# Performance work log

Measured on AMD Instinct MI355X. Metric: run time of the kernel, lower is better.

## Reference

```python
import jax, jax.numpy as jnp
import numpy as np

# Matcher weights (Deformable-DETR defaults used by SimPLR-style repos)
COST_CLASS, COST_BBOX, COST_GIOU = 2.0, 5.0, 2.0
ALPHA, GAMMA = 0.25, 2.0  # focal cost hyperparams
EPS = 1e-8


def box_cxcywh_to_xyxy(b):
    cx, cy, w, h = jnp.split(b, 4, axis=-1)
    return jnp.concatenate([cx - 0.5 * w, cy - 0.5 * h, cx + 0.5 * w, cy + 0.5 * h], axis=-1)


def generalized_box_iou(b1, b2):
    # b1 [Q,4], b2 [T,4] in xyxy -> [Q,T]
    area1 = (b1[:, 2] - b1[:, 0]) * (b1[:, 3] - b1[:, 1])
    area2 = (b2[:, 2] - b2[:, 0]) * (b2[:, 3] - b2[:, 1])
    lt = jnp.maximum(b1[:, None, :2], b2[None, :, :2])
    rb = jnp.minimum(b1[:, None, 2:], b2[None, :, 2:])
    wh = jnp.clip(rb - lt, 0.0)
    inter = wh[..., 0] * wh[..., 1]
    union = area1[:, None] + area2[None, :] - inter
    iou = inter / union
    lt2 = jnp.minimum(b1[:, None, :2], b2[None, :, :2])
    rb2 = jnp.maximum(b1[:, None, 2:], b2[None, :, 2:])
    wh2 = jnp.clip(rb2 - lt2, 0.0)
    hull = wh2[..., 0] * wh2[..., 1]
    return iou - (hull - union) / hull


def cost_matrix(logits, boxes, tgt_ids, tgt_boxes):
    # per-image: logits [Q,C], boxes [Q,4] cxcywh, tgt_ids [T], tgt_boxes [T,4]
    prob = jax.nn.sigmoid(logits)
    neg = (1.0 - ALPHA) * (prob ** GAMMA) * (-jnp.log(1.0 - prob + EPS))
    pos = ALPHA * ((1.0 - prob) ** GAMMA) * (-jnp.log(prob + EPS))
    cost_class = pos[:, tgt_ids] - neg[:, tgt_ids]                    # [Q,T]
    cost_bbox = jnp.abs(boxes[:, None, :] - tgt_boxes[None, :, :]).sum(-1)  # L1 cdist [Q,T]
    cost_giou = -generalized_box_iou(box_cxcywh_to_xyxy(boxes), box_cxcywh_to_xyxy(tgt_boxes))
    return COST_BBOX * cost_bbox + COST_CLASS * cost_class + COST_GIOU * cost_giou


def lsa(cost):
    # Hungarian (Jonker-Volgenant / e-maxx shortest augmenting path), minimizes.
    # cost [n, m] with n <= m; returns col4row: column assigned to each row.
    n, m = cost.shape
    u = np.zeros(n + 1)
    v = np.zeros(m + 1)
    p = np.zeros(m + 1, dtype=np.int64)   # p[j] = row matched to col j (1-based), 0 = free
    way = np.zeros(m + 1, dtype=np.int64)
    for i in range(1, n + 1):
        p[0] = i
        j0 = 0
        minv = np.full(m + 1, np.inf)
        used = np.zeros(m + 1, dtype=bool)
        while True:
            used[j0] = True
            i0 = p[j0]
            free = ~used
            free[0] = False
            cur = cost[i0 - 1] - u[i0] - v[1:]
            better = np.zeros(m + 1, dtype=bool)
            better[1:] = free[1:] & (cur < minv[1:])
            minv[better] = cur[better[1:]]
            way[better] = j0
            cand = np.where(free[1:], minv[1:], np.inf)
            j1 = int(np.argmin(cand)) + 1
            delta = cand[j1 - 1]
            u[p[used]] += delta
            v[used] -= delta
            minv[free] -= delta
            j0 = j1
            if p[j0] == 0:
                break
        while j0 != 0:
            j1 = way[j0]
            p[j0] = p[j1]
            j0 = j1
    col4row = np.zeros(n, dtype=np.int64)
    for j in range(1, m + 1):
        if p[j] > 0:
            col4row[p[j] - 1] = j - 1
    return col4row


_batched_cost = jax.jit(jax.vmap(cost_matrix, in_axes=(0, 0, 0, 0)))


def setup_inputs() -> dict:
    key = jax.random.key(0)
    k1, k2, k3, k4 = jax.random.split(key, 4)
    bs, nq, nc, nt = 32, 900, 1203, 100
    return {
        "pred_logits": jax.random.normal(k1, (bs, nq, nc), dtype=jnp.float32),
        "pred_boxes": jax.random.uniform(k2, (bs, nq, 4), dtype=jnp.float32),
        "tgt_labels": jax.random.randint(k3, (bs, nt), 0, nc, dtype=jnp.int64),
        "tgt_boxes": jax.random.uniform(k4, (bs, nt, 4), dtype=jnp.float32),
    }


def reference(pred_logits, pred_boxes, tgt_labels, tgt_boxes):
    # Cost blocks [bs, Q, T] (identical to the per-image diagonal blocks of the
    # torch code's [bs, Q, sum_T] view, which are the only parts used).
    C = _batched_cost(pred_logits, pred_boxes, tgt_labels, tgt_boxes)
    Cn = np.asarray(jax.device_get(C))
    rows, cols = [], []
    for b in range(Cn.shape[0]):
        col4row = lsa(Cn[b].T)          # [T]: matched query index per target
        order = np.argsort(col4row)     # scipy returns row indices sorted ascending
        rows.append(col4row[order])     # index_i: selected prediction indices
        cols.append(order)              # index_j: corresponding target indices
    pred_idx = jnp.asarray(np.stack(rows), dtype=jnp.int64)  # [bs, T]
    tgt_idx = jnp.asarray(np.stack(cols), dtype=jnp.int64)   # [bs, T]
    return C, pred_idx, tgt_idx
```

## Files before the change

### kernel.cpp

```cpp
#include <hip/hip_runtime.h>
#include <math.h>

#define BS 32
#define NQ 900
#define NC 1203
#define NT 100
#define SLOTS 15
#define K8 8
#define JBLK 512
#define NW 8

__device__ float g_CT[(size_t)BS * NT * NQ];
__device__ unsigned long long g_topk[(size_t)BS * NT * K8];

__device__ __forceinline__ unsigned long long packf(float f, int col) {
    unsigned k = __float_as_uint(f);
    k = (k & 0x80000000u) ? ~k : (k | 0x80000000u);
    return ((unsigned long long)k << 32) | (unsigned)col;
}
__device__ __forceinline__ float unpack_val(unsigned long long p) {
    unsigned k = (unsigned)(p >> 32);
    unsigned bits = (k & 0x80000000u) ? (k ^ 0x80000000u) : ~k;
    return __uint_as_float(bits);
}
__device__ __forceinline__ int unpack_col(unsigned long long p) {
    return (int)(p & 0xFFFFFFFFu);
}

__global__ __launch_bounds__(128) void cost_kernel(
    const float* __restrict__ logits, const float* __restrict__ boxes,
    const int* __restrict__ tlabels, const float* __restrict__ tboxes,
    float* __restrict__ C)
{
    int bq = blockIdx.x;
    int b = bq / NQ, q = bq % NQ;
    int t = threadIdx.x;

    const float* pb = boxes + (size_t)(b * NQ + q) * 4;
    float pcx = pb[0], pcy = pb[1], pw = pb[2], ph = pb[3];

    if (t < NT) {
        int id = tlabels[b * NT + t];
        float x = logits[(size_t)(b * NQ + q) * NC + id];
        float prob = 1.0f / (1.0f + expf(-x));
        float neg = 0.75f * (prob * prob) * (-logf(1.0f - prob + 1e-8f));
        float pos = 0.25f * ((1.0f - prob) * (1.0f - prob)) * (-logf(prob + 1e-8f));
        float cclass = pos - neg;

        const float* tb = tboxes + (size_t)(b * NT + t) * 4;
        float tcx = tb[0], tcy = tb[1], tw = tb[2], th = tb[3];
        float cbbox = fabsf(pcx - tcx) + fabsf(pcy - tcy) + fabsf(pw - tw) + fabsf(ph - th);

        float p0 = pcx - 0.5f * pw, p1 = pcy - 0.5f * ph;
        float p2 = pcx + 0.5f * pw, p3 = pcy + 0.5f * ph;
        float t0 = tcx - 0.5f * tw, t1 = tcy - 0.5f * th;
        float t2 = tcx + 0.5f * tw, t3 = tcy + 0.5f * th;
        float area1 = (p2 - p0) * (p3 - p1);
        float area2 = (t2 - t0) * (t3 - t1);
        float ltx = fmaxf(p0, t0), lty = fmaxf(p1, t1);
        float rbx = fminf(p2, t2), rby = fminf(p3, t3);
        float wx = fmaxf(rbx - ltx, 0.0f), wy = fmaxf(rby - lty, 0.0f);
        float inter = wx * wy;
        float uni = area1 + area2 - inter;
        float iou = inter / uni;
        float l2x = fminf(p0, t0), l2y = fminf(p1, t1);
        float r2x = fmaxf(p2, t2), r2y = fmaxf(p3, t3);
        float hx = fmaxf(r2x - l2x, 0.0f), hy = fmaxf(r2y - l2y, 0.0f);
        float hull = hx * hy;
        float giou = iou - (hull - uni) / hull;

        C[(size_t)(b * NQ + q) * NT + t] =
            5.0f * cbbox + 2.0f * cclass + 2.0f * (-giou);
    }
}

__global__ __launch_bounds__(256) void transpose_kernel(const float* __restrict__ C)
{
    __shared__ float tile[64][101];
    int b = blockIdx.x / 15;
    int chunk = blockIdx.x % 15;
    int q0 = chunk * 64;
    int nq = (q0 + 64 <= NQ) ? 64 : (NQ - q0);
    int tid = threadIdx.x;

    const float* Cb = C + (size_t)b * NQ * NT;
    for (int e = tid; e < nq * NT; e += 256) {
        int qq = e / NT, t = e % NT;
        tile[qq][t] = Cb[(size_t)(q0 + qq) * NT + t];
    }
    __syncthreads();
    float* CTb = g_CT + (size_t)b * NT * NQ;
    for (int e = tid; e < NT * nq; e += 256) {
        int t = e / nq, qq = e % nq;
        CTb[(size_t)t * NQ + q0 + qq] = tile[qq][t];
    }
}

__global__ __launch_bounds__(64) void topk_kernel()
{
    int bi = blockIdx.x;
    const float* row = g_CT + (size_t)bi * NQ;
    int lane = threadIdx.x;

    unsigned long long r[K8];
    #pragma unroll
    for (int m = 0; m < K8; ++m) r[m] = 0xFFFFFFFFFFFFFFFFull;

    #pragma unroll
    for (int k = 0; k < SLOTS; ++k) {
        int j = (k << 6) + lane;
        if ((k < SLOTS - 1) || (j < NQ)) {
            unsigned long long key = packf(row[j], j);
            #pragma unroll
            for (int m = 0; m < K8; ++m) {
                unsigned long long lo = key < r[m] ? key : r[m];
                unsigned long long hi = key < r[m] ? r[m] : key;
                r[m] = lo; key = hi;
            }
        }
    }
    #pragma unroll
    for (int off = 32; off; off >>= 1) {
        unsigned long long bv[K8], tmp[K8];
        #pragma unroll
        for (int m = 0; m < K8; ++m) bv[m] = __shfl_down(r[m], off);
        #pragma unroll
        for (int m = 0; m < K8; ++m) {
            unsigned long long x = bv[K8 - 1 - m];
            tmp[m] = r[m] < x ? r[m] : x;
        }
        #pragma unroll
        for (int d = 4; d; d >>= 1) {
            #pragma unroll
            for (int m = 0; m < K8; ++m) {
                if (!(m & d)) {
                    unsigned long long a = tmp[m], b2 = tmp[m | d];
                    tmp[m] = a < b2 ? a : b2;
                    tmp[m | d] = a < b2 ? b2 : a;
                }
            }
        }
        #pragma unroll
        for (int m = 0; m < K8; ++m) r[m] = tmp[m];
    }
    if (lane == 0) {
        #pragma unroll
        for (int m = 0; m < K8; ++m) g_topk[(size_t)bi * K8 + m] = r[m];
    }
}

__global__ __launch_bounds__(JBLK) void jv_kernel(
    const float* __restrict__ C,
    float* __restrict__ pred_out, float* __restrict__ tgt_out)
{
    int b = blockIdx.x;
    const float* Cb = C + (size_t)b * NQ * NT;
    int tid = threadIdx.x;
    int w = tid >> 6, lane = tid & 63;
    const double INF = __builtin_huge_val();

    __shared__ double u[NT];
    __shared__ double vsh[NQ];
    __shared__ double distA[128];
    __shared__ int pathA[128];
    __shared__ int asgCols[128];
    __shared__ int pos4col[NQ];
    __shared__ int row4col[NQ];
    __shared__ int col4row[NT];
    __shared__ int aminsh[NT];
    __shared__ int freeRows[NT + 2 * NW];
    __shared__ int parked[NT];
    __shared__ int srList[140];
    __shared__ unsigned long long tksh[NT][K8];
    __shared__ unsigned char visits[NT];
    __shared__ double pm1[NW], pm2[NW];
    __shared__ int pj1[NW], prow[NW];
    __shared__ int nFreeSh, nParkSh, asgCountSh;

    for (int j = tid; j < NQ; j += JBLK) { vsh[j] = 0.0; row4col[j] = 0x7fffffff; pos4col[j] = -1; }
    {
        const unsigned long long* src = g_topk + (size_t)b * NT * K8;
        for (int e = tid; e < NT * K8; e += JBLK) ((unsigned long long*)tksh)[e] = src[e];
    }
    for (int i = tid; i < NT; i += JBLK) { col4row[i] = -1; visits[i] = 0; }
    if (tid == 0) { nFreeSh = 0; nParkSh = 0; asgCountSh = 0; }
    __syncthreads();
    for (int i = tid; i < NT; i += JBLK) {
        unsigned long long tk = tksh[i][0];
        aminsh[i] = unpack_col(tk);
        u[i] = (double)unpack_val(tk);
    }
    __syncthreads();

    for (int i = tid; i < NT; i += JBLK) atomicMin(&row4col[aminsh[i]], i);
    __syncthreads();
    if (tid == 0) {
        int n = 0, cnt = 0;
        for (int i = 0; i < NT; ++i) {
            int j = aminsh[i];
            if (row4col[j] == i) { col4row[i] = j; pos4col[j] = cnt; asgCols[cnt++] = j; }
            else freeRows[n++] = i;
        }
        nFreeSh = n; asgCountSh = cnt;
    }
    __syncthreads();
    for (int j = tid; j < NQ; j += JBLK)
        if (row4col[j] == 0x7fffffff) row4col[j] = -1;
    __syncthreads();

    int guard = 0;
    while (guard++ < 250) {
        int nf = nFreeSh;
        if (nf == 0) break;
        int take = nf < NW ? nf : NW;
        if (w < take) {
            int i = freeRows[nf - 1 - w];
            int asgCount = asgCountSh;

            double m1 = INF, m2 = INF; int j1 = -1;
            bool haveFree = (lane < K8) && (row4col[unpack_col(tksh[i][lane])] < 0);
            unsigned long long bal = __ballot(haveFree);
            if (__popcll(bal) >= 2) {
                #pragma unroll
                for (int s = 0; s < 2; ++s) {
                    int pos = lane + (s << 6);
                    if (pos < asgCount) {
                        int j = asgCols[pos];
                        double cur = (double)Cb[(size_t)j * NT + i] - vsh[j];
                        if (cur < m1) { m2 = m1; m1 = cur; j1 = j; }
                        else if (cur < m2) m2 = cur;
                    }
                }
                if (haveFree) {
                    unsigned long long tk = tksh[i][lane];
                    double cur = (double)unpack_val(tk);
                    int j = unpack_col(tk);
                    if (cur < m1) { m2 = m1; m1 = cur; j1 = j; }
                    else if (cur < m2) m2 = cur;
                }
            } else {
                #pragma unroll
                for (int k = 0; k < SLOTS; ++k) {
                    int j = (k << 6) + lane;
                    if ((k < SLOTS - 1) || (j < NQ)) {
                        double cur = (double)Cb[(size_t)j * NT + i] - vsh[j];
                        if (cur < m1) { m2 = m1; m1 = cur; j1 = j; }
                        else if (cur < m2) m2 = cur;
                    }
                }
            }
            for (int off = 32; off; off >>= 1) {
                double o1 = __shfl_down(m1, off); int oj = __shfl_down(j1, off);
                double o2 = __shfl_down(m2, off);
                if (o1 < m1 || (o1 == m1 && (unsigned)oj < (unsigned)j1)) { m2 = fmin(m1, o2); m1 = o1; j1 = oj; }
                else m2 = fmin(m2, o1);
            }
            if (lane == 0) { pm1[w] = m1; pm2[w] = m2; pj1[w] = j1; prow[w] = i; }
        }
        __syncthreads();
        if (tid == 0) {
            int n = nf - take;
            int cj[NW]; int nc = 0;
            for (int k = 0; k < take; ++k) {
                int i = prow[k];
                if (visits[i] >= 2) { parked[nParkSh] = i; nParkSh++; continue; }
                int j1 = pj1[k];
                bool clash = false;
                for (int k2 = 0; k2 < nc; ++k2) if (cj[k2] == j1) clash = true;
                if (clash) { freeRows[n++] = i; continue; }
                cj[nc++] = j1;
                visits[i]++;
                double m1 = pm1[k], m2 = pm2[k];
                u[i] = m2;
                vsh[j1] -= (m2 - m1);
                int inc = row4col[j1];
                row4col[j1] = i; col4row[i] = j1;
                if (inc >= 0) { col4row[inc] = -1; freeRows[n++] = inc; }
                else { pos4col[j1] = asgCountSh; asgCols[asgCountSh] = j1; asgCountSh++; }
            }
            nFreeSh = n;
        }
        __syncthreads();
    }
    if (tid == 0) {
        while (nFreeSh > 0) { nFreeSh--; parked[nParkSh] = freeRows[nFreeSh]; nParkSh++; }
    }
    __syncthreads();

    int np = nParkSh;
    for (int f = 0; f < np; ++f) {
        int curRow = parked[f];
        int asgCount = asgCountSh;
        double mvA = INF, mvB = INF;
        bool pA = false, pB = false;
        double bestFree = INF; int bfCol = -1, bfRow = -1;
        double minVal = 0.0; int i = curRow; int nSr = 1;
        if (w == 0) {
            for (int pos = lane; pos < asgCount; pos += 64) distA[pos] = INF;
            if (lane == 0) srList[0] = curRow;
        }
        __syncthreads();

        if (w == 0) {
            int g2 = 0; bool sink = false;
            while (!sink && g2++ < 120) {
                double ui = u[i];
                {
                    int pos = lane;
                    if (pos < asgCount && !pA) {
                        int j = asgCols[pos];
                        double cur = minVal + (double)Cb[(size_t)j * NT + i] - ui - vsh[j];
                        if (cur < mvA) { mvA = cur; distA[pos] = cur; pathA[pos] = i; }
                    }
                    pos = lane + 64;
                    if (pos < asgCount && !pB) {
                        int j = asgCols[pos];
                        double cur = minVal + (double)Cb[(size_t)j * NT + i] - ui - vsh[j];
                        if (cur < mvB) { mvB = cur; distA[pos] = cur; pathA[pos] = i; }
                    }
                }
                double fc = INF; int fj = -1;
                if (lane < K8) {
                    unsigned long long tk = tksh[i][lane];
                    int j = unpack_col(tk);
                    if (row4col[j] < 0) { fc = minVal + (double)unpack_val(tk) - ui; fj = j; }
                }
                if (__ballot(fc < INF) == 0ull) {
                    #pragma unroll
                    for (int k = 0; k < SLOTS; ++k) {
                        int j = (k << 6) + lane;
                        if (((k < SLOTS - 1) || (j < NQ)) && row4col[j] < 0) {
                            double cur = minVal + (double)Cb[(size_t)j * NT + i] - ui;
                            if (cur < fc) { fc = cur; fj = j; }
                        }
                    }
                }
                double pv; int ppos;
                double pva = pA ? INF : mvA, pvb = pB ? INF : mvB;
                if (pvb < pva) { pv = pvb; ppos = lane + 64; } else { pv = pva; ppos = lane; }
                for (int off = 32; off; off >>= 1) {
                    double o = __shfl_down(pv, off); int op = __shfl_down(ppos, off);
                    if (o < pv || (o == pv && op < ppos)) { pv = o; ppos = op; }
                    double of = __shfl_down(fc, off); int ofj = __shfl_down(fj, off);
                    if (of < fc || (of == fc && (unsigned)ofj < (unsigned)fj)) { fc = of; fj = ofj; }
                }
                pv = __shfl(pv, 0); ppos = __shfl(ppos, 0);
                fc = __shfl(fc, 0); fj = __shfl(fj, 0);
                if (fc < bestFree) { bestFree = fc; bfCol = fj; bfRow = i; }
                if (bestFree <= pv) { minVal = bestFree; sink = true; }
                else {
                    minVal = pv;
                    if (lane == (ppos & 63)) { if (ppos < 64) pA = true; else pB = true; }
                    i = row4col[asgCols[ppos]];
                    if (lane == 0) srList[nSr] = i;
                    nSr++;
                }
            }
            if (lane == 0) { pm1[0] = minVal; pj1[0] = bfCol; prow[0] = bfRow; pm2[0] = (double)nSr; }
        }
        __syncthreads();

        if (tid == 0) {
            double mv = pm1[0]; int ns = (int)pm2[0];
            u[curRow] += mv;
            for (int t2 = 1; t2 < ns; ++t2) {
                int ri = srList[t2];
                u[ri] += mv - distA[pos4col[col4row[ri]]];
            }
        }
        if (w == 0) {
            double mv = pm1[0];
            int pos = lane;
            if (pos < asgCount && pA) vsh[asgCols[pos]] -= mv - distA[pos];
            pos = lane + 64;
            if (pos < asgCount && pB) vsh[asgCols[pos]] -= mv - distA[pos];
        }
        if (tid == 0) {
            int j = pj1[0], ri = prow[0]; int g3 = 0;
            while (g3++ < 128) {
                row4col[j] = ri;
                int tj = col4row[ri]; col4row[ri] = j;
                if (ri == curRow) break;
                j = tj; ri = pathA[pos4col[j]];
            }
            pos4col[pj1[0]] = asgCountSh; asgCols[asgCountSh] = pj1[0]; asgCountSh++;
        }
        __syncthreads();
    }

    for (int i2 = tid; i2 < NT; i2 += JBLK) {
        int ci = col4row[i2];
        int rank = 0;
        for (int k2 = 0; k2 < NT; ++k2) rank += (col4row[k2] < ci);
        pred_out[b * NT + rank] = (float)ci;
        tgt_out[b * NT + rank] = (float)i2;
    }
}

extern "C" void kernel_launch(void* const* d_in, const int* in_sizes, int n_in,
                              void* d_out, int out_size, void* d_ws, size_t ws_size,
                              hipStream_t stream) {
    const float* logits = (const float*)d_in[0];
    const float* boxes  = (const float*)d_in[1];
    const int*   tlab   = (const int*)d_in[2];
    const float* tboxes = (const float*)d_in[3];

    float* out  = (float*)d_out;
    float* C    = out;
    float* pred = out + (size_t)BS * NQ * NT;
    float* tgt  = pred + BS * NT;

    cost_kernel<<<BS * NQ, 128, 0, stream>>>(logits, boxes, tlab, tboxes, C);
    transpose_kernel<<<BS * 15, 256, 0, stream>>>(C);
    topk_kernel<<<BS * NT, 64, 0, stream>>>();
    jv_kernel<<<BS, JBLK, 0, stream>>>(C, pred, tgt);
}
```

Baseline: 91.36 us.

## Cache assigned-column cost rows in LDS and compact column duals

Keeps the cost rows of the assigned columns in a shared-memory tile (padded to 101 to avoid bank conflicts) and stores column duals only for assigned columns, indexed by position. The auction and augmenting-path inner loops then read LDS instead of scattered global loads. New columns are copied into the tile after each round, which adds an extra block barrier per iteration and uses about 50KB of LDS.

```diff
diff --git a/kernel.cpp b/kernel.cpp
--- a/kernel.cpp
+++ b/kernel.cpp
@@ -9,6 +9,7 @@
 #define K8 8
 #define JBLK 512
 #define NW 8
+#define ACAP 128
 
 __device__ float g_CT[(size_t)BS * NT * NQ];
 __device__ unsigned long long g_topk[(size_t)BS * NT * K8];
@@ -159,11 +160,12 @@
     int w = tid >> 6, lane = tid & 63;
     const double INF = __builtin_huge_val();
 
+    __shared__ float asgLds[ACAP][101];
+    __shared__ double vAsg[ACAP];
     __shared__ double u[NT];
-    __shared__ double vsh[NQ];
-    __shared__ double distA[128];
-    __shared__ int pathA[128];
-    __shared__ int asgCols[128];
+    __shared__ double distA[ACAP];
+    __shared__ int pathA[ACAP];
+    __shared__ int asgCols[ACAP];
     __shared__ int pos4col[NQ];
     __shared__ int row4col[NQ];
     __shared__ int col4row[NT];
@@ -175,9 +177,14 @@
     __shared__ unsigned char visits[NT];
     __shared__ double pm1[NW], pm2[NW];
     __shared__ int pj1[NW], prow[NW];
-    __shared__ int nFreeSh, nParkSh, asgCountSh;
-
-    for (int j = tid; j < NQ; j += JBLK) { vsh[j] = 0.0; row4col[j] = 0x7fffffff; pos4col[j] = -1; }
+    __shared__ int nFreeSh, nParkSh, asgCountSh, oldCntSh;
+
+    auto vOf = [&](int j) -> double {
+        int p = pos4col[j];
+        return (p >= 0) ? vAsg[p] : 0.0;
+    };
+
+    for (int j = tid; j < NQ; j += JBLK) { row4col[j] = 0x7fffffff; pos4col[j] = -1; }
     {
         const unsigned long long* src = g_topk + (size_t)b * NT * K8;
         for (int e = tid; e < NT * K8; e += JBLK) ((unsigned long long*)tksh)[e] = src[e];
@@ -206,6 +213,14 @@
     __syncthreads();
     for (int j = tid; j < NQ; j += JBLK)
         if (row4col[j] == 0x7fffffff) row4col[j] = -1;
+    {
+        int cnt = asgCountSh;
+        for (int p = tid; p < cnt; p += JBLK) vAsg[p] = 0.0;
+        for (int e = tid; e < cnt * NT; e += JBLK) {
+            int pos = e / NT, i = e - pos * NT;
+            asgLds[pos][i] = Cb[(size_t)asgCols[pos] * NT + i];
+        }
+    }
     __syncthreads();
 
     int guard = 0;
@@ -225,8 +240,8 @@
                 for (int s = 0; s < 2; ++s) {
                     int pos = lane + (s << 6);
                     if (pos < asgCount) {
+                        double cur = (double)asgLds[pos][i] - vAsg[pos];
                         int j = asgCols[pos];
-                        double cur = (double)Cb[(size_t)j * NT + i] - vsh[j];
                         if (cur < m1) { m2 = m1; m1 = cur; j1 = j; }
                         else if (cur < m2) m2 = cur;
                     }
@@ -243,7 +258,7 @@
                 for (int k = 0; k < SLOTS; ++k) {
                     int j = (k << 6) + lane;
                     if ((k < SLOTS - 1) || (j < NQ)) {
-                        double cur = (double)Cb[(size_t)j * NT + i] - vsh[j];
+                        double cur = (double)Cb[(size_t)j * NT + i] - vOf(j);
                         if (cur < m1) { m2 = m1; m1 = cur; j1 = j; }
                         else if (cur < m2) m2 = cur;
                     }
@@ -260,6 +275,7 @@
         __syncthreads();
         if (tid == 0) {
             int n = nf - take;
+            int oldCnt = asgCountSh;
             int cj[NW]; int nc = 0;
             for (int k = 0; k < take; ++k) {
                 int i = prow[k];
@@ -272,13 +288,27 @@
                 visits[i]++;
                 double m1 = pm1[k], m2 = pm2[k];
                 u[i] = m2;
-                vsh[j1] -= (m2 - m1);
                 int inc = row4col[j1];
                 row4col[j1] = i; col4row[i] = j1;
-                if (inc >= 0) { col4row[inc] = -1; freeRows[n++] = inc; }
-                else { pos4col[j1] = asgCountSh; asgCols[asgCountSh] = j1; asgCountSh++; }
-            }
-            nFreeSh = n;
+                if (inc >= 0) {
+                    vAsg[pos4col[j1]] -= (m2 - m1);
+                    col4row[inc] = -1; freeRows[n++] = inc;
+                } else {
+                    int cnt = asgCountSh;
+                    pos4col[j1] = cnt; asgCols[cnt] = j1;
+                    vAsg[cnt] = -(m2 - m1);
+                    asgCountSh = cnt + 1;
+                }
+            }
+            nFreeSh = n; oldCntSh = oldCnt;
+        }
+        __syncthreads();
+        {
+            int from = oldCntSh, to = asgCountSh;
+            for (int e = tid; e < (to - from) * NT; e += JBLK) {
+                int pos = from + e / NT, i = e - (e / NT) * NT;
+                asgLds[pos][i] = Cb[(size_t)asgCols[pos] * NT + i];
+            }
         }
         __syncthreads();
     }
@@ -308,14 +338,12 @@
                 {
                     int pos = lane;
                     if (pos < asgCount && !pA) {
-                        int j = asgCols[pos];
-                        double cur = minVal + (double)Cb[(size_t)j * NT + i] - ui - vsh[j];
+                        double cur = minVal + (double)asgLds[pos][i] - ui - vAsg[pos];
                         if (cur < mvA) { mvA = cur; distA[pos] = cur; pathA[pos] = i; }
                     }
                     pos = lane + 64;
                     if (pos < asgCount && !pB) {
-                        int j = asgCols[pos];
-                        double cur = minVal + (double)Cb[(size_t)j * NT + i] - ui - vsh[j];
+                        double cur = minVal + (double)asgLds[pos][i] - ui - vAsg[pos];
                         if (cur < mvB) { mvB = cur; distA[pos] = cur; pathA[pos] = i; }
                     }
                 }
@@ -371,9 +399,9 @@
         if (w == 0) {
             double mv = pm1[0];
             int pos = lane;
-            if (pos < asgCount && pA) vsh[asgCols[pos]] -= mv - distA[pos];
+            if (pos < asgCount && pA) vAsg[pos] -= mv - distA[pos];
             pos = lane + 64;
-            if (pos < asgCount && pB) vsh[asgCols[pos]] -= mv - distA[pos];
+            if (pos < asgCount && pB) vAsg[pos] -= mv - distA[pos];
         }
         if (tid == 0) {
             int j = pj1[0], ri = prow[0]; int g3 = 0;
@@ -383,7 +411,18 @@
                 if (ri == curRow) break;
                 j = tj; ri = pathA[pos4col[j]];
             }
-            pos4col[pj1[0]] = asgCountSh; asgCols[asgCountSh] = pj1[0]; asgCountSh++;
+            int cnt = asgCountSh;
+            pos4col[pj1[0]] = cnt; asgCols[cnt] = pj1[0];
+            vAsg[cnt] = 0.0;
+            oldCntSh = cnt; asgCountSh = cnt + 1;
+        }
+        __syncthreads();
+        {
+            int from = oldCntSh, to = asgCountSh;
+            for (int e = tid; e < (to - from) * NT; e += JBLK) {
+                int pos = from + e / NT, i2 = e - (e / NT) * NT;
+                asgLds[pos][i2] = Cb[(size_t)asgCols[pos] * NT + i2];
+            }
         }
         __syncthreads();
     }
```

New measurement: 93.62 us. 2.5% more time.
